# Optimization experiments

Measured on AMD Instinct MI355X. Metric: run time of the kernel, lower is better.

The kernel has to match this reference:

```python
import jax, jax.numpy as jnp
import numpy as np

B, S, D, H, DH = 2, 2048, 1024, 16, 64
R_ATTN, R_OUT, I, R_FC1, R_FC2 = 32, 512, 4096, 512, 512
LN_EPS = 1e-5


def _layernorm(x, g, b):
    mu = jnp.mean(x, axis=-1, keepdims=True)
    var = jnp.mean(jnp.square(x - mu), axis=-1, keepdims=True)
    return (x - mu) * jax.lax.rsqrt(var + LN_EPS) * g + b


def setup_inputs() -> dict:
    key = jax.random.key(0)
    ks = jax.random.split(key, 16)
    std = 0.02
    return {
        'hidden_states': jax.random.normal(ks[0], (B, S, D), jnp.float32),
        'ln1_g': jnp.ones((D,), jnp.float32),
        'ln1_b': jnp.zeros((D,), jnp.float32),
        'ln2_g': jnp.ones((D,), jnp.float32),
        'ln2_b': jnp.zeros((D,), jnp.float32),
        'q_U': jax.random.normal(ks[1], (D, H, R_ATTN), jnp.float32) * std,
        'q_V': jax.random.normal(ks[2], (H, R_ATTN, DH), jnp.float32) * std,
        'q_b': jnp.zeros((H, DH), jnp.float32),
        'k_U': jax.random.normal(ks[3], (D, H, R_ATTN), jnp.float32) * std,
        'k_V': jax.random.normal(ks[4], (H, R_ATTN, DH), jnp.float32) * std,
        'k_b': jnp.zeros((H, DH), jnp.float32),
        'v_U': jax.random.normal(ks[5], (D, H, R_ATTN), jnp.float32) * std,
        'v_V': jax.random.normal(ks[6], (H, R_ATTN, DH), jnp.float32) * std,
        'v_b': jnp.zeros((H, DH), jnp.float32),
        'out_U': jax.random.normal(ks[7], (D, R_OUT), jnp.float32) * std,
        'out_V': jax.random.normal(ks[8], (R_OUT, D), jnp.float32) * std,
        'out_b': jnp.zeros((D,), jnp.float32),
        'fc1_U': jax.random.normal(ks[9], (D, R_FC1), jnp.float32) * std,
        'fc1_V': jax.random.normal(ks[10], (R_FC1, I), jnp.float32) * std,
        'fc1_b': jnp.zeros((I,), jnp.float32),
        'fc2_U': jax.random.normal(ks[11], (I, R_FC2), jnp.float32) * std,
        'fc2_V': jax.random.normal(ks[12], (R_FC2, D), jnp.float32) * std,
        'fc2_b': jnp.zeros((D,), jnp.float32),
    }


def reference(hidden_states, ln1_g, ln1_b, ln2_g, ln2_b,
              q_U, q_V, q_b, k_U, k_V, k_b, v_U, v_V, v_b,
              out_U, out_V, out_b, fc1_U, fc1_V, fc1_b, fc2_U, fc2_V, fc2_b):
    Bx, Sx, Dx = hidden_states.shape
    scale = 1.0 / np.sqrt(DH).astype(np.float32)
    x = _layernorm(hidden_states, ln1_g, ln1_b)
    # low-rank per-head QKV: [B,S,D]x[D,H,r]x[H,r,dh] -> [B,H,S,dh]
    Q = jnp.einsum('bsd,dhr,hre->bhse', x, q_U, q_V) + q_b[None, :, None, :]
    K = jnp.einsum('bsd,dhr,hre->bhse', x, k_U, k_V) + k_b[None, :, None, :]
    V = jnp.einsum('bsd,dhr,hre->bhse', x, v_U, v_V) + v_b[None, :, None, :]
    scores = jnp.einsum('bhse,bhte->bhst', Q, K) * scale  # [B,H,S,S]
    causal = jnp.tril(jnp.ones((Sx, Sx), bool))
    neg_inf = jnp.finfo(scores.dtype).min
    scores = jnp.where(causal, scores, neg_inf)
    probs = jax.nn.softmax(scores, axis=-1)
    Y = jnp.einsum('bhst,bhte->bhse', probs, V)
    Y = Y.transpose(0, 2, 1, 3).reshape(Bx, Sx, Dx)  # merge heads
    Y = (Y @ out_U) @ out_V + out_b
    h = hidden_states + Y
    z = _layernorm(h, ln2_g, ln2_b)
    h1 = jax.nn.gelu((z @ fc1_U) @ fc1_V + fc1_b, approximate=False)
    h2 = (h1 @ fc2_U) @ fc2_V + fc2_b
    return h + h2
```

## Files before the change

### kernel.cpp

```cpp
#include <hip/hip_runtime.h>
#include <cstdint>
#include <cstddef>


#define NTOK 4096
#define DM   1024
#define SEQ  2048

typedef __attribute__((ext_vector_type(8))) __bf16 bf16x8;
typedef __attribute__((ext_vector_type(4))) __bf16 bf16x4;
typedef __attribute__((ext_vector_type(4))) float  f32x4;

__device__ __forceinline__ f32x4 mfma16(bf16x8 a, bf16x8 b, f32x4 c) {
  return __builtin_amdgcn_mfma_f32_16x16x32_bf16(a, b, c, 0, 0, 0);
}

__device__ __forceinline__ void gload16(const __bf16* g, __bf16* l) {
  __builtin_amdgcn_global_load_lds(
      (const __attribute__((address_space(1))) void*)g,
      (__attribute__((address_space(3))) void*)l, 16, 0, 0);
}

__device__ __forceinline__ void xcd_map(int flat, int gx, int gy,
                                        int BM, int BN, int& bm, int& bn) {
  int nwg = gx * gy;
  if ((nwg & 7) == 0) flat = (flat & 7) * (nwg >> 3) + (flat >> 3);
  bm = (flat / gx) * BM;
  bn = (flat % gx) * BN;
}

__global__ __launch_bounds__(256) void transpose_k(const float* __restrict__ in,
                                                   __bf16* __restrict__ out,
                                                   int R, int C) {
  __shared__ __bf16 t[32][33];
  int tx = threadIdx.x & 31, ty = threadIdx.x >> 5;
  int r0 = blockIdx.y * 32, c0 = blockIdx.x * 32;
#pragma unroll
  for (int i = 0; i < 32; i += 8)
    t[ty + i][tx] = (__bf16)in[(size_t)(r0 + ty + i) * C + c0 + tx];
  __syncthreads();
#pragma unroll
  for (int i = 0; i < 32; i += 8)
    out[(size_t)(c0 + ty + i) * R + r0 + tx] = t[tx][ty + i];
}

__global__ __launch_bounds__(256) void prep_k(
    const float* __restrict__ qb, const float* __restrict__ kb,
    const float* __restrict__ vb, float* __restrict__ bqkv,
    const float* __restrict__ outU, __bf16* __restrict__ outUT,
    const float* __restrict__ outV, __bf16* __restrict__ outVT,
    const float* __restrict__ f1U,  __bf16* __restrict__ f1UT,
    const float* __restrict__ f1V,  __bf16* __restrict__ f1VT,
    const float* __restrict__ f2V,  __bf16* __restrict__ f2VT,
    const float* __restrict__ f2U,  __bf16* __restrict__ f2UT,
    __bf16* __restrict__ outUc) {
  int blk = blockIdx.x;
  if (blk < 12) {
    int i = blk * 256 + threadIdx.x;
    bqkv[i] = (i < 1024) ? qb[i] : (i < 2048 ? kb[i - 1024] : vb[i - 2048]);
    return;
  }
  int t = blk - 12;
  if (t >= 6144) {
    int i = (t - 6144) * 2048 + threadIdx.x * 8;
    float4 a = *(const float4*)(outU + i);
    float4 b = *(const float4*)(outU + i + 4);
    bf16x8 o = {(__bf16)a.x, (__bf16)a.y, (__bf16)a.z, (__bf16)a.w,
                (__bf16)b.x, (__bf16)b.y, (__bf16)b.z, (__bf16)b.w};
    *(bf16x8*)(outUc + i) = o;
    return;
  }
  const float* in; __bf16* out; int R, C;
  if (t < 512)       { in = outU; out = outUT; R = 1024; C = 512;  }
  else if (t < 1024) { in = outV; out = outVT; R = 512;  C = 1024; t -= 512; }
  else if (t < 1536) { in = f1U;  out = f1UT;  R = 1024; C = 512;  t -= 1024; }
  else if (t < 3584) { in = f1V;  out = f1VT;  R = 512;  C = 4096; t -= 1536; }
  else if (t < 4096) { in = f2V;  out = f2VT;  R = 512;  C = 1024; t -= 3584; }
  else               { in = f2U;  out = f2UT;  R = 4096; C = 512;  t -= 4096; }
  int ct = C >> 5;
  int c0 = (t % ct) * 32, r0 = (t / ct) * 32;
  __shared__ __bf16 tt[32][33];
  int tx = threadIdx.x & 31, ty = threadIdx.x >> 5;
#pragma unroll
  for (int i = 0; i < 32; i += 8)
    tt[ty + i][tx] = (__bf16)in[(size_t)(r0 + ty + i) * C + c0 + tx];
  __syncthreads();
#pragma unroll
  for (int i = 0; i < 32; i += 8)
    out[(size_t)(c0 + ty + i) * R + r0 + tx] = tt[tx][ty + i];
}

__global__ __launch_bounds__(256) void trans_v(const __bf16* __restrict__ qkv,
                                               __bf16* __restrict__ VT) {
  __shared__ __bf16 t[32][33];
  int tx = threadIdx.x & 31, ty = threadIdx.x >> 5;
  int bh = blockIdx.z, b = bh >> 4, h = bh & 15;
  int k0 = blockIdx.x * 32, d0 = blockIdx.y * 32;
#pragma unroll
  for (int i = 0; i < 32; i += 8)
    t[ty + i][tx] = qkv[(size_t)(b * SEQ + k0 + ty + i) * 3072 + 2048 + h * 64 + d0 + tx];
  __syncthreads();
#pragma unroll
  for (int i = 0; i < 32; i += 8)
    VT[(size_t)(bh * 64 + d0 + ty + i) * SEQ + k0 + tx] = t[tx][ty + i];
}

__global__ __launch_bounds__(256) void combine_uv(const float* __restrict__ qU,
                                                  const float* __restrict__ qV,
                                                  const float* __restrict__ kU,
                                                  const float* __restrict__ kV,
                                                  const float* __restrict__ vU,
                                                  const float* __restrict__ vV,
                                                  __bf16* __restrict__ WT) {
  __shared__ float sV[2048];
  int tid = threadIdx.x;
  int blk = blockIdx.x;
  int sel = blk >> 7;
  int rem = blk & 127;
  int h = rem >> 3, dc = rem & 7;
  int d0 = dc << 7;
  const float* U = sel == 0 ? qU : (sel == 1 ? kU : vU);
  const float* V = sel == 0 ? qV : (sel == 1 ? kV : vV);
  for (int i = tid; i < 2048; i += 256) sV[i] = V[h * 2048 + i];
  int d = d0 + (tid & 127);
  int eh = tid >> 7;
  const float* up = U + (size_t)d * 512 + h * 32;
  float u[32];
#pragma unroll
  for (int i = 0; i < 8; i++)
    *(float4*)&u[i * 4] = *(const float4*)(up + i * 4);
  __syncthreads();
  int e0 = eh * 32;
#pragma unroll
  for (int eg = 0; eg < 8; eg++) {
    float ax = 0.f, ay = 0.f, az = 0.f, aw = 0.f;
#pragma unroll
    for (int r = 0; r < 32; r++) {
      float4 v4 = *(const float4*)&sV[r * 64 + e0 + eg * 4];
      ax += u[r] * v4.x; ay += u[r] * v4.y;
      az += u[r] * v4.z; aw += u[r] * v4.w;
    }
    size_t prow = (size_t)(sel * 1024 + h * 64 + e0 + eg * 4) * 1024 + d;
    WT[prow]        = (__bf16)ax;
    WT[prow + 1024] = (__bf16)ay;
    WT[prow + 2048] = (__bf16)az;
    WT[prow + 3072] = (__bf16)aw;
  }
}

__global__ __launch_bounds__(256) void cast_k(const float* __restrict__ in,
                                              __bf16* __restrict__ out, int n) {
  int i = blockIdx.x * 256 + threadIdx.x;
  if (i < n) out[i] = (__bf16)in[i];
}

__global__ __launch_bounds__(256) void merge4_k(const float* __restrict__ p,
                                                __bf16* __restrict__ out) {
  int i = blockIdx.x * 256 + threadIdx.x;
  float s = (p[i] + p[i + 2097152]) + (p[i + 4194304] + p[i + 6291456]);
  out[i] = (__bf16)s;
}

template <int TWO>
__global__ __launch_bounds__(256) void ln_k(const float* __restrict__ x,
                                            const __bf16* __restrict__ x2,
                                            const float* __restrict__ g,
                                            const float* __restrict__ b,
                                            __bf16* __restrict__ out) {
  int row = blockIdx.x, tid = threadIdx.x;
  int c = tid * 4;
  float4 v4 = *(const float4*)(x + (size_t)row * DM + c);
  float v[4] = {v4.x, v4.y, v4.z, v4.w};
  if (TWO) {
    bf16x4 e = *(const bf16x4*)(x2 + (size_t)row * DM + c);
    v[0] += (float)e[0]; v[1] += (float)e[1];
    v[2] += (float)e[2]; v[3] += (float)e[3];
  }
  float s  = (v[0] + v[1]) + (v[2] + v[3]);
  float ss = (v[0] * v[0] + v[1] * v[1]) + (v[2] * v[2] + v[3] * v[3]);
#pragma unroll
  for (int m = 1; m < 64; m <<= 1) { s += __shfl_xor(s, m); ss += __shfl_xor(ss, m); }
  __shared__ float rs_[4], rss[4];
  if ((tid & 63) == 0) { rs_[tid >> 6] = s; rss[tid >> 6] = ss; }
  __syncthreads();
  s  = (rs_[0] + rs_[1]) + (rs_[2] + rs_[3]);
  ss = (rss[0] + rss[1]) + (rss[2] + rss[3]);
  float mu  = s * (1.f / 1024.f);
  float var = ss * (1.f / 1024.f) - mu * mu;
  float rstd = rsqrtf(var + 1e-5f);
  float4 g4 = *(const float4*)(g + c);
  float4 b4 = *(const float4*)(b + c);
  bf16x4 o = {(__bf16)((v[0] - mu) * rstd * g4.x + b4.x),
              (__bf16)((v[1] - mu) * rstd * g4.y + b4.y),
              (__bf16)((v[2] - mu) * rstd * g4.z + b4.z),
              (__bf16)((v[3] - mu) * rstd * g4.w + b4.w)};
  *(bf16x4*)(out + (size_t)row * DM + c) = o;
}

template <int EPI, int BN>
__global__ __launch_bounds__(256) void gemm_bt(const __bf16* __restrict__ A,
                                               const __bf16* __restrict__ BT,
                                               void* __restrict__ Cv,
                                               const float* __restrict__ bias,
                                               const float* __restrict__ resF,
                                               const __bf16* __restrict__ resB,
                                               int M, int N, int K) {
  constexpr int WR = (BN == 128) ? 4 : 2;
  __shared__ alignas(16) __bf16 la[2][128 * 32];
  __shared__ alignas(16) __bf16 lb[2][BN * 32];
  int tid = threadIdx.x;
  int lane = tid & 63;
  int wave = tid >> 6;
  int quad = lane >> 4, l15 = lane & 15;
  int flat = blockIdx.y * gridDim.x + blockIdx.x;
  int bm, bn;
  xcd_map(flat, gridDim.x, gridDim.y, 128, BN, bm, bn);
  int wm = (BN == 128) ? (wave >> 1) * 64 : wave * 32;
  int wn = (BN == 128) ? (wave & 1) * 64 : 0;
  int lr = lane >> 2;
  int lc = (((lane & 3) ^ ((lr >> 1) & 3))) * 8;
  const __bf16* ga = A  + (size_t)(bm + wave * 32 + lr) * K + lc;
  const __bf16* gb = BT + (size_t)(bn + wave * (BN == 128 ? 32 : 16) + lr) * K + lc;
  int ksw = ((l15 >> 1) & 3) * 8;
  f32x4 acc[WR][4] = {};

  auto stage = [&](int k0, int b) {
    __bf16* lab = &la[b][wave * 1024];
    gload16(ga + k0, lab);
    gload16(ga + (size_t)16 * K + k0, lab + 512);
    if (BN == 128) {
      __bf16* lbb = &lb[b][wave * 1024];
      gload16(gb + k0, lbb);
      gload16(gb + (size_t)16 * K + k0, lbb + 512);
    } else {
      gload16(gb + k0, &lb[b][wave * 512]);
    }
  };

  stage(0, 0);
  __syncthreads();
  for (int k0 = 0; k0 < K; k0 += 32) {
    int b = (k0 >> 5) & 1;
    if (k0 + 32 < K) stage(k0 + 32, b ^ 1);
    bf16x8 af[WR], bfr[4];
#pragma unroll
    for (int i = 0; i < WR; i++)
      af[i] = *(const bf16x8*)&la[b][(wm + i * 16 + l15) * 32 + (quad * 8 ^ ksw)];
#pragma unroll
    for (int j = 0; j < 4; j++)
      bfr[j] = *(const bf16x8*)&lb[b][(wn + j * 16 + l15) * 32 + (quad * 8 ^ ksw)];
#pragma unroll
    for (int i = 0; i < WR; i++)
#pragma unroll
      for (int j = 0; j < 4; j++)
        acc[i][j] = mfma16(af[i], bfr[j], acc[i][j]);
    __syncthreads();
  }
#pragma unroll
  for (int i = 0; i < WR; i++) {
#pragma unroll
    for (int j = 0; j < 4; j++) {
      int col = bn + wn + j * 16 + l15;
      float bv = bias ? bias[col] : 0.f;
#pragma unroll
      for (int r = 0; r < 4; r++) {
        int row = bm + wm + i * 16 + quad * 4 + r;
        size_t idx = (size_t)row * N + col;
        float v = acc[i][j][r] + bv;
        if (EPI == 0) {
          ((__bf16*)Cv)[idx] = (__bf16)v;
        } else if (EPI == 1) {
          float y = 0.79788456080286536f * fmaf(0.044715f * v, v * v, v);
          float u = exp2f(y * 2.885390081777926f);
          float th = (u - 1.f) / (u + 1.f);
          v = 0.5f * v * (1.f + th);
          ((__bf16*)Cv)[idx] = (__bf16)v;
        } else {
          v += resF[idx] + (float)resB[idx];
          ((float*)Cv)[idx] = v;
        }
      }
    }
  }
}

__global__ __launch_bounds__(256) void gemm_bt64s(const __bf16* __restrict__ A,
                                                  const __bf16* __restrict__ BT,
                                                  __bf16* __restrict__ C,
                                                  int M, int N, int K) {
  __shared__ alignas(16) __bf16 la[2][64 * 32];
  __shared__ alignas(16) __bf16 lb[2][64 * 32];
  int tid = threadIdx.x;
  int lane = tid & 63;
  int wave = tid >> 6;
  int quad = lane >> 4, l15 = lane & 15;
  int flat = blockIdx.y * gridDim.x + blockIdx.x;
  int bm, bn;
  xcd_map(flat, gridDim.x, gridDim.y, 64, 64, bm, bn);
  int lr = tid >> 2;
  int lc = (((tid & 3) ^ ((lr >> 1) & 3))) * 8;
  const __bf16* ga = A  + (size_t)(bm + lr) * K + lc;
  const __bf16* gb = BT + (size_t)(bn + lr) * K + lc;
  int ksw = ((l15 >> 1) & 3) * 8;
  f32x4 acc[4] = {};

  auto stage = [&](int k0, int b) {
    gload16(ga + k0, &la[b][tid * 8]);
    gload16(gb + k0, &lb[b][tid * 8]);
  };

  stage(0, 0);
  __syncthreads();
  for (int k0 = 0; k0 < K; k0 += 32) {
    int b = (k0 >> 5) & 1;
    if (k0 + 32 < K) stage(k0 + 32, b ^ 1);
    bf16x8 af = *(const bf16x8*)&la[b][(wave * 16 + l15) * 32 + (quad * 8 ^ ksw)];
    bf16x8 bfr[4];
#pragma unroll
    for (int j = 0; j < 4; j++)
      bfr[j] = *(const bf16x8*)&lb[b][(j * 16 + l15) * 32 + (quad * 8 ^ ksw)];
#pragma unroll
    for (int j = 0; j < 4; j++)
      acc[j] = mfma16(af, bfr[j], acc[j]);
    __syncthreads();
  }
#pragma unroll
  for (int j = 0; j < 4; j++) {
    int col = bn + j * 16 + l15;
#pragma unroll
    for (int r = 0; r < 4; r++) {
      int row = bm + wave * 16 + quad * 4 + r;
      C[(size_t)row * N + col] = (__bf16)acc[j][r];
    }
  }
}

template <int ATOMIC>
__global__ __launch_bounds__(256) void gemm_sk(const __bf16* __restrict__ A,
                                               const __bf16* __restrict__ BT,
                                               float* __restrict__ Cf,
                                               int M, int N, int K, int KS) {
  __shared__ alignas(16) __bf16 la[2][128 * 32];
  __shared__ alignas(16) __bf16 lb[2][128 * 32];
  int tid = threadIdx.x;
  int lane = tid & 63;
  int wave = tid >> 6;
  int quad = lane >> 4, l15 = lane & 15;
  int flat = blockIdx.y * gridDim.x + blockIdx.x;
  int bm, bn;
  xcd_map(flat, gridDim.x, gridDim.y, 128, 128, bm, bn);
  int wm = (wave >> 1) * 64, wn = (wave & 1) * 64;
  int klen = K / KS;
  int kbeg = blockIdx.z * klen, kend = kbeg + klen;
  int lr = lane >> 2;
  int lc = (((lane & 3) ^ ((lr >> 1) & 3))) * 8;
  const __bf16* ga = A  + (size_t)(bm + wave * 32 + lr) * K + lc;
  const __bf16* gb = BT + (size_t)(bn + wave * 32 + lr) * K + lc;
  int ksw = ((l15 >> 1) & 3) * 8;
  f32x4 acc[4][4] = {};

  auto stage = [&](int k0, int b) {
    __bf16* lab = &la[b][wave * 1024];
    __bf16* lbb = &lb[b][wave * 1024];
    gload16(ga + k0, lab);
    gload16(ga + (size_t)16 * K + k0, lab + 512);
    gload16(gb + k0, lbb);
    gload16(gb + (size_t)16 * K + k0, lbb + 512);
  };

  stage(kbeg, 0);
  __syncthreads();
  for (int k0 = kbeg; k0 < kend; k0 += 32) {
    int b = ((k0 - kbeg) >> 5) & 1;
    if (k0 + 32 < kend) stage(k0 + 32, b ^ 1);
    bf16x8 af[4], bfr[4];
#pragma unroll
    for (int i = 0; i < 4; i++)
      af[i] = *(const bf16x8*)&la[b][(wm + i * 16 + l15) * 32 + (quad * 8 ^ ksw)];
#pragma unroll
    for (int j = 0; j < 4; j++)
      bfr[j] = *(const bf16x8*)&lb[b][(wn + j * 16 + l15) * 32 + (quad * 8 ^ ksw)];
#pragma unroll
    for (int i = 0; i < 4; i++)
#pragma unroll
      for (int j = 0; j < 4; j++)
        acc[i][j] = mfma16(af[i], bfr[j], acc[i][j]);
    __syncthreads();
  }
  float* out = ATOMIC ? Cf : Cf + (size_t)blockIdx.z * M * N;
#pragma unroll
  for (int i = 0; i < 4; i++)
#pragma unroll
    for (int j = 0; j < 4; j++) {
      int col = bn + wn + j * 16 + l15;
#pragma unroll
      for (int r = 0; r < 4; r++) {
        int row = bm + wm + i * 16 + quad * 4 + r;
        if (ATOMIC) atomicAdd(&out[(size_t)row * N + col], acc[i][j][r]);
        else        out[(size_t)row * N + col] = acc[i][j][r];
      }
    }
}

#define JOB(q, a, b) ((uint32_t)(q) | ((uint32_t)(a) << 8) | ((uint32_t)(b) << 16))
__device__ const uint32_t JOBTAB[24] = {
  JOB(7, 0, 16),  JOB(15, 0, 16), JOB(15, 16, 32),
  JOB(14, 0, 15), JOB(14, 15, 30),
  JOB(6, 0, 14),  JOB(13, 0, 14), JOB(13, 14, 28),
  JOB(12, 0, 13), JOB(12, 13, 26),
  JOB(5, 0, 12),  JOB(11, 0, 12), JOB(11, 12, 24),
  JOB(10, 0, 11), JOB(10, 11, 22),
  JOB(4, 0, 10),  JOB(9, 0, 10),  JOB(9, 10, 20),
  JOB(8, 0, 9),   JOB(8, 9, 18),
  JOB(3, 0, 8),   JOB(2, 0, 6),   JOB(1, 0, 4),   JOB(0, 0, 2),
};

__global__ __launch_bounds__(512, 6) void attn_k(const __bf16* __restrict__ QKV,
                                                 const __bf16* __restrict__ VT,
                                                 __bf16* __restrict__ Y,
                                                 float* __restrict__ Opart,
                                                 float* __restrict__ lpart) {
  const float SC = 0.18033688011112042f;
  const float C2 = 23.083120654223414f;
  __shared__ alignas(16) __bf16 lk[2][64 * 64];
  __shared__ alignas(16) __bf16 lv[2][64 * 64];
  __shared__ alignas(16) __bf16 P[8][16 * 72];
  int tid = threadIdx.x;
  int wave = tid >> 6, lane = tid & 63;
  int quad = lane >> 4, l15 = lane & 15;
  int bh = blockIdx.x & 31;
  int job = blockIdx.x >> 5;
  uint32_t jt = JOBTAB[job];
  int qb = jt & 255, kbeg = (jt >> 8) & 255, kend = (jt >> 16) & 255;
  bool split = qb >= 8;
  int b = bh >> 4, h = bh & 15;
  int q0w = (qb << 7) + wave * 16;
  const size_t RS = 3 * DM;
  const __bf16* base = QKV + (size_t)b * SEQ * RS;
  const __bf16* vtb  = VT + (size_t)bh * 64 * SEQ;

  const __bf16* qp = base + (size_t)(q0w + l15) * RS + h * 64 + quad * 8;
  bf16x8 aq0 = *(const bf16x8*)qp;
  bf16x8 aq1 = *(const bf16x8*)(qp + 32);

  int srow = tid >> 3, schunk = tid & 7;
  int sswz = (schunk ^ (srow & 7)) << 3;
  const __bf16* gk_src = base + (size_t)srow * RS + DM + h * 64 + sswz;
  const __bf16* gv_src = vtb + (size_t)srow * SEQ + sswz;

  int c0 = (quad ^ (l15 & 7)) << 3;
  int c1 = ((quad + 4) ^ (l15 & 7)) << 3;

  f32x4 zero4 = {0.f, 0.f, 0.f, 0.f};
  f32x4 O[4] = {zero4, zero4, zero4, zero4};
  float l_i = 0.f;

  int ntiles = kend - kbeg;

  gload16(gk_src + ((size_t)kbeg << 6) * RS, &lk[0][tid * 8]);
  gload16(gv_src + ((size_t)kbeg << 6),      &lv[0][tid * 8]);
  __syncthreads();

  for (int t = 0; t < ntiles; t++) {
    int kt = kbeg + t;
    int cur = t & 1;
    if (t + 1 < ntiles) {
      size_t kn = (size_t)(kt + 1) << 6;
      gload16(gk_src + kn * RS, &lk[cur ^ 1][tid * 8]);
      gload16(gv_src + kn,      &lv[cur ^ 1][tid * 8]);
    }
    int k0 = kt << 6;
    if (k0 <= q0w + 15) {
      f32x4 s[4] = {zero4, zero4, zero4, zero4};
#pragma unroll
      for (int gk = 0; gk < 4; gk++) {
        const __bf16* kr = &lk[cur][(gk * 16 + l15) * 64];
        bf16x8 kb0 = *(const bf16x8*)(kr + c0);
        bf16x8 kb1 = *(const bf16x8*)(kr + c1);
        s[gk] = mfma16(kb0, aq0, s[gk]);
        s[gk] = mfma16(kb1, aq1, s[gk]);
      }
      if (k0 + 63 <= q0w) {
#pragma unroll
        for (int gk = 0; gk < 4; gk++) {
          float p0 = exp2f(fmaf(s[gk][0], SC, -C2));
          float p1 = exp2f(fmaf(s[gk][1], SC, -C2));
          float p2 = exp2f(fmaf(s[gk][2], SC, -C2));
          float p3 = exp2f(fmaf(s[gk][3], SC, -C2));
          l_i += (p0 + p1) + (p2 + p3);
          bf16x4 pw = {(__bf16)p0, (__bf16)p1, (__bf16)p2, (__bf16)p3};
          *(bf16x4*)&P[wave][l15 * 72 + gk * 16 + quad * 4] = pw;
        }
      } else {
        int qrow = q0w + l15;
#pragma unroll
        for (int gk = 0; gk < 4; gk++) {
          int kb = k0 + gk * 16 + quad * 4;
          float p0 = (kb     <= qrow) ? exp2f(fmaf(s[gk][0], SC, -C2)) : 0.f;
          float p1 = (kb + 1 <= qrow) ? exp2f(fmaf(s[gk][1], SC, -C2)) : 0.f;
          float p2 = (kb + 2 <= qrow) ? exp2f(fmaf(s[gk][2], SC, -C2)) : 0.f;
          float p3 = (kb + 3 <= qrow) ? exp2f(fmaf(s[gk][3], SC, -C2)) : 0.f;
          l_i += (p0 + p1) + (p2 + p3);
          bf16x4 pw = {(__bf16)p0, (__bf16)p1, (__bf16)p2, (__bf16)p3};
          *(bf16x4*)&P[wave][l15 * 72 + gk * 16 + quad * 4] = pw;
        }
      }
      bf16x8 ap0 = *(const bf16x8*)&P[wave][l15 * 72 + quad * 8];
      bf16x8 ap1 = *(const bf16x8*)&P[wave][l15 * 72 + 32 + quad * 8];
#pragma unroll
      for (int nt = 0; nt < 4; nt++) {
        const __bf16* vr = &lv[cur][(nt * 16 + l15) * 64];
        bf16x8 bv0 = *(const bf16x8*)(vr + c0);
        bf16x8 bv1 = *(const bf16x8*)(vr + c1);
        O[nt] = mfma16(ap0, bv0, O[nt]);
        O[nt] = mfma16(ap1, bv1, O[nt]);
      }
    }
    __syncthreads();
  }

  l_i += __shfl_xor(l_i, 16);
  l_i += __shfl_xor(l_i, 32);
  if (!split) {
#pragma unroll
    for (int r = 0; r < 4; r++) {
      float inv = 1.f / __shfl(l_i, quad * 4 + r);
      size_t orow = (size_t)(b * SEQ + q0w + quad * 4 + r);
      __bf16* yp = Y + orow * DM + h * 64 + l15;
      yp[0]  = (__bf16)(O[0][r] * inv);
      yp[16] = (__bf16)(O[1][r] * inv);
      yp[32] = (__bf16)(O[2][r] * inv);
      yp[48] = (__bf16)(O[3][r] * inv);
    }
  } else {
#pragma unroll
    for (int r = 0; r < 4; r++) {
      int row = (q0w - 1024) + quad * 4 + r;
      float* op = Opart + (((size_t)bh << 10) + row) * 64 + l15;
      atomicAdd(op +  0, O[0][r]);
      atomicAdd(op + 16, O[1][r]);
      atomicAdd(op + 32, O[2][r]);
      atomicAdd(op + 48, O[3][r]);
    }
    if (quad == 0)
      atomicAdd(&lpart[((size_t)bh << 10) + (q0w - 1024) + l15], l_i);
  }
}

__global__ __launch_bounds__(256) void norm_k(const float* __restrict__ Op,
                                              const float* __restrict__ lp,
                                              __bf16* __restrict__ Y) {
  int idx = blockIdx.x * 256 + threadIdx.x;
  int dh = idx & 63;
  int row = (idx >> 6) & 1023;
  int bh = idx >> 16;
  int b = bh >> 4, h = bh & 15;
  float inv = 1.f / lp[(bh << 10) + row];
  Y[(size_t)(b * SEQ + 1024 + row) * DM + h * 64 + dh] = (__bf16)(Op[idx] * inv);
}

extern "C" void kernel_launch(void* const* d_in, const int* in_sizes, int n_in,
                              void* d_out, int out_size, void* d_ws, size_t ws_size,
                              hipStream_t stream) {
  (void)in_sizes; (void)n_in; (void)out_size;
  const float* hidden = (const float*)d_in[0];
  const float* ln1_g  = (const float*)d_in[1];
  const float* ln1_b  = (const float*)d_in[2];
  const float* ln2_g  = (const float*)d_in[3];
  const float* ln2_b  = (const float*)d_in[4];
  const float* q_U = (const float*)d_in[5];
  const float* q_V = (const float*)d_in[6];
  const float* q_b = (const float*)d_in[7];
  const float* k_U = (const float*)d_in[8];
  const float* k_V = (const float*)d_in[9];
  const float* k_b = (const float*)d_in[10];
  const float* v_U = (const float*)d_in[11];
  const float* v_V = (const float*)d_in[12];
  const float* v_b = (const float*)d_in[13];
  const float* out_U = (const float*)d_in[14];
  const float* out_V = (const float*)d_in[15];
  const float* out_b = (const float*)d_in[16];
  const float* fc1_U = (const float*)d_in[17];
  const float* fc1_V = (const float*)d_in[18];
  const float* fc1_b = (const float*)d_in[19];
  const float* fc2_U = (const float*)d_in[20];
  const float* fc2_V = (const float*)d_in[21];
  const float* fc2_b = (const float*)d_in[22];

  const size_t MB = 1u << 20;
  char* ws = (char*)d_ws;
  bool big = ws_size >= 128 * MB;
  __bf16* outUT = (__bf16*)(ws + 0 * MB);
  __bf16* outVT = (__bf16*)(ws + 1 * MB);
  __bf16* f1UT  = (__bf16*)(ws + 2 * MB);
  __bf16* f1VT  = (__bf16*)(ws + 3 * MB);
  __bf16* f2VT  = (__bf16*)(ws + 7 * MB);
  float*  bqkv  = (float*) (ws + 8 * MB);
  __bf16* wqkvT = (__bf16*)(ws + 9 * MB);
  __bf16* f2UT  = big ? (__bf16*)(ws + 55 * MB)
                      : (__bf16*)(ws + 9 * MB);
  __bf16* xln   = (__bf16*)(ws + 15 * MB);
  __bf16* yattn = (__bf16*)(ws + 15 * MB);
  __bf16* zbuf  = (__bf16*)(ws + 15 * MB);
  float*  t3f32 = (float*) (ws + 15 * MB);
  __bf16* t3bf  = (__bf16*)(ws + 19 * MB);
  __bf16* qkv   = (__bf16*)(ws + 23 * MB);
  __bf16* h1c   = big ? (__bf16*)(ws + 64 * MB)
                      : (__bf16*)(ws + 23 * MB);
  float*  t3p   = (float*) (ws + 96 * MB);
  __bf16* tbuf  = (__bf16*)(ws + 43 * MB);
  __bf16* VT    = (__bf16*)(ws + 47 * MB);
  __bf16* hres  = (__bf16*)(ws + 47 * MB);
  __bf16* WoutT = (__bf16*)(ws + 59 * MB);
  __bf16* outUc = (__bf16*)(ws + 61 * MB);
  float* Opart = (float*)d_out;
  float* lpart = (float*)d_out + 2097152;

  prep_k<<<big ? 6412 : 4108, 256, 0, stream>>>(
      q_b, k_b, v_b, bqkv, out_U, outUT, out_V, outVT,
      fc1_U, f1UT, fc1_V, f1VT, fc2_V, f2VT, fc2_U, f2UT, outUc);
  combine_uv<<<384, 256, 0, stream>>>(q_U, q_V, k_U, k_V, v_U, v_V, wqkvT);
  if (big)
    gemm_bt<0, 64><<<dim3(16, 8), 256, 0, stream>>>(outVT, outUc, WoutT,
                                                    nullptr, nullptr, nullptr,
                                                    1024, 1024, 512);

  ln_k<0><<<NTOK, 256, 0, stream>>>(hidden, nullptr, ln1_g, ln1_b, xln);
  gemm_bt<0, 128><<<dim3(24, 32), 256, 0, stream>>>(xln, wqkvT, qkv, bqkv,
                                                    nullptr, nullptr, NTOK, 3072, 1024);
  if (!big)
    transpose_k<<<dim3(16, 128), 256, 0, stream>>>(fc2_U, f2UT, 4096, 512);
  trans_v<<<dim3(64, 2, 32), 256, 0, stream>>>(qkv, VT);
  hipMemsetAsync(d_out, 0, (size_t)8519680, stream);
  attn_k<<<768, 512, 0, stream>>>(qkv, VT, yattn, Opart, lpart);
  norm_k<<<8192, 256, 0, stream>>>(Opart, lpart, yattn);
  if (big) {
    gemm_bt<0, 64><<<dim3(16, 32), 256, 0, stream>>>(yattn, WoutT, hres, out_b,
                                                     nullptr, nullptr, NTOK, 1024, 1024);
  } else {
    gemm_bt64s<<<dim3(8, 64), 256, 0, stream>>>(yattn, outUT, tbuf, NTOK, 512, 1024);
    gemm_bt<0, 64><<<dim3(16, 32), 256, 0, stream>>>(tbuf, outVT, hres, out_b,
                                                     nullptr, nullptr, NTOK, 1024, 512);
  }
  ln_k<1><<<NTOK, 256, 0, stream>>>(hidden, hres, ln2_g, ln2_b, zbuf);
  gemm_bt64s<<<dim3(8, 64), 256, 0, stream>>>(zbuf, f1UT, tbuf, NTOK, 512, 1024);
  if (big) {
    gemm_bt<1, 128><<<dim3(32, 32), 256, 0, stream>>>(tbuf, f1VT, h1c, fc1_b,
                                                      nullptr, nullptr, NTOK, 4096, 512);
    gemm_sk<0><<<dim3(4, 32, 4), 256, 0, stream>>>(h1c, f2UT, t3p,
                                                   NTOK, 512, 4096, 4);
    merge4_k<<<8192, 256, 0, stream>>>(t3p, t3bf);
  } else {
    for (int mc = 0; mc < 2; mc++) {
      __bf16* tchunk = tbuf + (size_t)mc * 2048 * 512;
      gemm_bt<1, 128><<<dim3(32, 16), 256, 0, stream>>>(tchunk, f1VT, h1c, fc1_b,
                                                        nullptr, nullptr, 2048, 4096, 512);
      hipMemsetAsync(t3f32, 0, (size_t)2048 * 512 * 4, stream);
      gemm_sk<1><<<dim3(4, 16, 4), 256, 0, stream>>>(h1c, f2UT, t3f32,
                                                     2048, 512, 4096, 4);
      cast_k<<<4096, 256, 0, stream>>>(t3f32, t3bf + (size_t)mc * 2048 * 512,
                                       2048 * 512);
    }
  }
  gemm_bt<3, 64><<<dim3(16, 32), 256, 0, stream>>>(t3bf, f2VT, (float*)d_out, fc2_b,
                                                   hidden, hres, NTOK, 1024, 512);
}
```

Baseline: 370.2 us.

## Fuse V transpose into QKV GEMM epilogue and fold prep work into existing kernels

In the big-workspace path, the QKV GEMM epilogue now writes V directly in transposed layout, which removes the separate trans_v kernel. The memset of the attention partial buffers moves into prep_k as zero-stores, replacing the outU bf16 copy. The out_U·out_V weight product is now computed in fp32 by extra combine_uv blocks instead of a bf16 MFMA GEMM launch. Together this removes several kernel launches and intermediate passes, at the cost of a scalar fp32 weight-combine and scattered 8-byte stores in the GEMM epilogue.

```diff
diff --git a/kernel.cpp b/kernel.cpp
--- a/kernel.cpp
+++ b/kernel.cpp
@@ -53,7 +53,7 @@
     const float* __restrict__ f1V,  __bf16* __restrict__ f1VT,
     const float* __restrict__ f2V,  __bf16* __restrict__ f2VT,
     const float* __restrict__ f2U,  __bf16* __restrict__ f2UT,
-    __bf16* __restrict__ outUc) {
+    float* __restrict__ zbuf) {
   int blk = blockIdx.x;
   if (blk < 12) {
     int i = blk * 256 + threadIdx.x;
@@ -63,11 +63,9 @@
   int t = blk - 12;
   if (t >= 6144) {
     int i = (t - 6144) * 2048 + threadIdx.x * 8;
-    float4 a = *(const float4*)(outU + i);
-    float4 b = *(const float4*)(outU + i + 4);
-    bf16x8 o = {(__bf16)a.x, (__bf16)a.y, (__bf16)a.z, (__bf16)a.w,
-                (__bf16)b.x, (__bf16)b.y, (__bf16)b.z, (__bf16)b.w};
-    *(bf16x8*)(outUc + i) = o;
+    float4 z = {0.f, 0.f, 0.f, 0.f};
+    *(float4*)(zbuf + i) = z;
+    *(float4*)(zbuf + i + 4) = z;
     return;
   }
   const float* in; __bf16* out; int R, C;
@@ -111,10 +109,42 @@
                                                   const float* __restrict__ kV,
                                                   const float* __restrict__ vU,
                                                   const float* __restrict__ vV,
-                                                  __bf16* __restrict__ WT) {
-  __shared__ float sV[2048];
+                                                  __bf16* __restrict__ WT,
+                                                  const float* __restrict__ oU,
+                                                  const float* __restrict__ oV,
+                                                  __bf16* __restrict__ WoutT) {
   int tid = threadIdx.x;
   int blk = blockIdx.x;
+  if (blk >= 384) {
+    __shared__ float sVW[128 * 32];
+    int t = blk - 384;
+    int k0 = (t >> 5) * 128, n0 = (t & 31) * 32;
+    int k = k0 + (tid & 127);
+    int nh = tid >> 7;
+    float acc[16] = {};
+    for (int rs = 0; rs < 4; rs++) {
+      __syncthreads();
+      for (int i = tid; i < 4096; i += 256)
+        sVW[i] = oV[(size_t)(rs * 128 + (i >> 5)) * 1024 + n0 + (i & 31)];
+      __syncthreads();
+      const float* up = oU + (size_t)k * 512 + rs * 128;
+#pragma unroll 8
+      for (int rr = 0; rr < 128; rr += 4) {
+        float4 u4 = *(const float4*)(up + rr);
+#pragma unroll
+        for (int j = 0; j < 16; j++) {
+          int nn = nh * 16 + j;
+          acc[j] += u4.x * sVW[(rr + 0) * 32 + nn] + u4.y * sVW[(rr + 1) * 32 + nn]
+                  + u4.z * sVW[(rr + 2) * 32 + nn] + u4.w * sVW[(rr + 3) * 32 + nn];
+        }
+      }
+    }
+#pragma unroll
+    for (int j = 0; j < 16; j++)
+      WoutT[(size_t)(n0 + nh * 16 + j) * 1024 + k] = (__bf16)acc[j];
+    return;
+  }
+  __shared__ float sV[2048];
   int sel = blk >> 7;
   int rem = blk & 127;
   int h = rem >> 3, dc = rem & 7;
@@ -262,12 +292,21 @@
     for (int j = 0; j < 4; j++) {
       int col = bn + wn + j * 16 + l15;
       float bv = bias ? bias[col] : 0.f;
+      if (EPI == 4 && col >= 2048) {
+        int rowb = bm + wm + i * 16 + quad * 4;
+        int bh = (rowb >> 11) * 16 + ((col - 2048) >> 6);
+        bf16x4 pv = {(__bf16)(acc[i][j][0] + bv), (__bf16)(acc[i][j][1] + bv),
+                     (__bf16)(acc[i][j][2] + bv), (__bf16)(acc[i][j][3] + bv)};
+        __bf16* vt = (__bf16*)resB;
+        *(bf16x4*)(vt + (size_t)(bh * 64 + (col & 63)) * SEQ + (rowb & 2047)) = pv;
+        continue;
+      }
 #pragma unroll
       for (int r = 0; r < 4; r++) {
         int row = bm + wm + i * 16 + quad * 4 + r;
         size_t idx = (size_t)row * N + col;
         float v = acc[i][j][r] + bv;
-        if (EPI == 0) {
+        if (EPI == 0 || EPI == 4) {
           ((__bf16*)Cv)[idx] = (__bf16)v;
         } else if (EPI == 1) {
           float y = 0.79788456080286536f * fmaf(0.044715f * v, v * v, v);
@@ -612,26 +651,26 @@
   __bf16* VT    = (__bf16*)(ws + 47 * MB);
   __bf16* hres  = (__bf16*)(ws + 47 * MB);
   __bf16* WoutT = (__bf16*)(ws + 59 * MB);
-  __bf16* outUc = (__bf16*)(ws + 61 * MB);
   float* Opart = (float*)d_out;
   float* lpart = (float*)d_out + 2097152;
 
-  prep_k<<<big ? 6412 : 4108, 256, 0, stream>>>(
+  prep_k<<<big ? 7196 : 4108, 256, 0, stream>>>(
       q_b, k_b, v_b, bqkv, out_U, outUT, out_V, outVT,
-      fc1_U, f1UT, fc1_V, f1VT, fc2_V, f2VT, fc2_U, f2UT, outUc);
-  combine_uv<<<384, 256, 0, stream>>>(q_U, q_V, k_U, k_V, v_U, v_V, wqkvT);
-  if (big)
-    gemm_bt<0, 64><<<dim3(16, 8), 256, 0, stream>>>(outVT, outUc, WoutT,
-                                                    nullptr, nullptr, nullptr,
-                                                    1024, 1024, 512);
+      fc1_U, f1UT, fc1_V, f1VT, fc2_V, f2VT, fc2_U, f2UT, (float*)d_out);
+  combine_uv<<<big ? 640 : 384, 256, 0, stream>>>(q_U, q_V, k_U, k_V, v_U, v_V,
+                                                  wqkvT, out_U, out_V, WoutT);
 
   ln_k<0><<<NTOK, 256, 0, stream>>>(hidden, nullptr, ln1_g, ln1_b, xln);
-  gemm_bt<0, 128><<<dim3(24, 32), 256, 0, stream>>>(xln, wqkvT, qkv, bqkv,
-                                                    nullptr, nullptr, NTOK, 3072, 1024);
-  if (!big)
+  if (big) {
+    gemm_bt<4, 128><<<dim3(24, 32), 256, 0, stream>>>(xln, wqkvT, qkv, bqkv,
+                                                      nullptr, VT, NTOK, 3072, 1024);
+  } else {
+    gemm_bt<0, 128><<<dim3(24, 32), 256, 0, stream>>>(xln, wqkvT, qkv, bqkv,
+                                                      nullptr, nullptr, NTOK, 3072, 1024);
     transpose_k<<<dim3(16, 128), 256, 0, stream>>>(fc2_U, f2UT, 4096, 512);
-  trans_v<<<dim3(64, 2, 32), 256, 0, stream>>>(qkv, VT);
-  hipMemsetAsync(d_out, 0, (size_t)8519680, stream);
+    trans_v<<<dim3(64, 2, 32), 256, 0, stream>>>(qkv, VT);
+    hipMemsetAsync(d_out, 0, (size_t)8519680, stream);
+  }
   attn_k<<<768, 512, 0, stream>>>(qkv, VT, yattn, Opart, lpart);
   norm_k<<<8192, 256, 0, stream>>>(Opart, lpart, yattn);
   if (big) {
```

Result: slower. 411.0 us (+11.0%).
